# Kernel tuning notes

Hardware: AMD Instinct MI355X
Metric: run time of the kernel (lower is better)

## Reference

```python
import jax, jax.numpy as jnp
import numpy as np

QBITS = 8
QMIN, QMAX = -(2 ** (QBITS - 1)), 2 ** (QBITS - 1) - 1  # qint8: -128..127


def fq_act(x):
    """Per-tensor affine fake-quant (observer = min/max of tensor), with STE."""
    mn = jnp.minimum(jnp.min(x), 0.0)
    mx = jnp.maximum(jnp.max(x), 0.0)
    scale = jnp.maximum((mx - mn) / (QMAX - QMIN), 1e-8)
    zp = QMIN - jnp.round(mn / scale)
    q = jnp.clip(jnp.round(x / scale) + zp, QMIN, QMAX)
    y = (q - zp) * scale
    return x + jax.lax.stop_gradient(y - x)


def fq_w(w):
    """Per-tensor symmetric weight fake-quant, with STE."""
    scale = jnp.maximum(jnp.max(jnp.abs(w)) / QMAX, 1e-8)
    y = jnp.clip(jnp.round(w / scale), QMIN, QMAX) * scale
    return w + jax.lax.stop_gradient(y - w)


def setup_inputs() -> dict:
    key = jax.random.key(0)
    ks = jax.random.split(key, 8)
    B, T, F, K = 32, 1024, 512, 31
    return {
        "x": jax.random.normal(ks[0], (B, T, F), jnp.float32),
        "ln_scale": jnp.ones((F,), jnp.float32),
        "ln_bias": jnp.zeros((F,), jnp.float32),
        "w1": jax.random.normal(ks[1], (2 * F, F), jnp.float32) * 0.02,
        "b1": jax.random.normal(ks[2], (2 * F,), jnp.float32) * 0.02,
        "dw_w": jax.random.normal(ks[3], (F, 1, K), jnp.float32) * 0.1,
        "dw_b": jax.random.normal(ks[4], (F,), jnp.float32) * 0.02,
        "bn_gamma": jnp.ones((F,), jnp.float32),
        "bn_beta": jnp.zeros((F,), jnp.float32),
        "bn_mean": jnp.zeros((F,), jnp.float32),
        "bn_var": jax.random.uniform(ks[5], (F,), jnp.float32, 0.5, 1.5),
        "w2": jax.random.normal(ks[6], (F, F), jnp.float32) * 0.02,
        "b2": jax.random.normal(ks[7], (F,), jnp.float32) * 0.02,
    }


def reference(x, ln_scale, ln_bias, w1, b1, dw_w, dw_b,
              bn_gamma, bn_beta, bn_mean, bn_var, w2, b2):
    F = x.shape[-1]
    # --- custom L1 layer norm, fake-quant in/out ---
    t = fq_act(x)
    t = t - jnp.mean(t, axis=-1, keepdims=True)
    t = t / (jnp.sum(jnp.abs(t), axis=-1, keepdims=True) / F + 1e-5)
    t = t * ln_scale + ln_bias
    t = fq_act(t)
    # --- pointwise conv 1 (linear F -> 2F), quant-wrapped ---
    t = fq_act(t)
    t = jnp.einsum("btf,of->bto", t, fq_w(w1)) + b1
    t = fq_act(t)
    # --- GLU, quant-wrapped ---
    t = fq_act(t)
    a, g = jnp.split(t, 2, axis=-1)
    t = a * jax.nn.sigmoid(g)
    t = fq_act(t)
    # --- depthwise conv over time, quant-wrapped ---
    t = jnp.transpose(t, (0, 2, 1))  # [B,F,T]
    t = fq_act(t)
    t = jax.lax.conv_general_dilated(
        t, fq_w(dw_w), window_strides=(1,), padding=[((dw_w.shape[-1] - 1) // 2,) * 2],
        dimension_numbers=("NCH", "OIH", "NCH"), feature_group_count=F,
    ) + dw_b[:, None]
    t = fq_act(t)
    # --- batch norm (eval mode, running stats), quant-wrapped ---
    t = fq_act(t)
    t = (t - bn_mean[:, None]) * (bn_gamma[:, None] / jnp.sqrt(bn_var[:, None] + 1e-5)) + bn_beta[:, None]
    t = fq_act(t)
    t = jnp.transpose(t, (0, 2, 1))  # [B,T,F]
    # --- SiLU activation, quant-wrapped ---
    t = fq_act(t)
    t = jax.nn.silu(t)
    t = fq_act(t)
    # --- pointwise conv 2 (linear F -> F), quant-wrapped ---
    t = fq_act(t)
    t = jnp.einsum("btf,of->bto", t, fq_w(w2)) + b2
    t = fq_act(t)
    return t  # dropout is identity at eval
```

## Files before the change

kernel.cpp:

```cpp
#include <hip/hip_runtime.h>
#include <stdint.h>
#include <math.h>

#define INF __builtin_inff()

typedef __attribute__((ext_vector_type(4))) float f32x4;
typedef __attribute__((ext_vector_type(2))) float f32x2;
typedef __attribute__((ext_vector_type(8))) short s16x8;

#define S_XMN 0
#define S_XMX 1
#define S_T1MN 2
#define S_T1MX 3
#define S_T4MN 4
#define S_T4MX 5
#define S_T7MN 6
#define S_T7MX 7
#define S_CVMN 8
#define S_CVMX 9
#define S_BNMN 10
#define S_BNMX 11
#define S_SIMN 12
#define S_SIMX 13
#define S_T18MN 14
#define S_T18MX 15
#define S_W1 16
#define S_W2 17
#define S_DW 18
#define NSLOT 19

#define NTOT 16777216L
#define TP 1056

__device__ __forceinline__ unsigned enc(float f) {
  unsigned u = __float_as_uint(f);
  return (u & 0x80000000u) ? ~u : (u | 0x80000000u);
}
__device__ __forceinline__ float dec(unsigned k) {
  return (k & 0x80000000u) ? __uint_as_float(k & 0x7FFFFFFFu) : __uint_as_float(~k);
}

struct FQ { float s, zp; };

__device__ __forceinline__ FQ fq_params(float mn_t, float mx_t) {
  float mn = fminf(mn_t, 0.0f), mx = fmaxf(mx_t, 0.0f);
  FQ p;
  p.s = fmaxf((mx - mn) / 255.0f, 1e-8f);
  p.zp = -128.0f - rintf(mn / p.s);
  return p;
}
__device__ __forceinline__ float fq_apply(float x, FQ p) {
  float q = rintf(x / p.s) + p.zp;
  q = fminf(fmaxf(q, -128.0f), 127.0f);
  return (q - p.zp) * p.s;
}
__device__ __forceinline__ float fq_qmz(float x, FQ p) {
  float q = rintf(x / p.s) + p.zp;
  q = fminf(fmaxf(q, -128.0f), 127.0f);
  return q - p.zp;
}
__device__ __forceinline__ void fq_pair(const unsigned* slots, int idx, FQ& p1, FQ& p2) {
  float mn = dec(slots[idx]), mx = dec(slots[idx + 1]);
  p1 = fq_params(mn, mx);
  float ymn = fq_apply(mn, p1), ymx = fq_apply(mx, p1);
  p2 = fq_params(ymn, ymx);
}
__device__ __forceinline__ unsigned short to_bf16(float v) {
  return (unsigned short)(__float_as_uint(v) >> 16);
}
__device__ __forceinline__ float from_bf16(unsigned short u) {
  return __uint_as_float(((unsigned)u) << 16);
}

__device__ __forceinline__ void mm_block_atomic(float mn, float mx, unsigned* smn, unsigned* smx) {
#pragma unroll
  for (int o = 32; o > 0; o >>= 1) {
    mn = fminf(mn, __shfl_down(mn, o, 64));
    mx = fmaxf(mx, __shfl_down(mx, o, 64));
  }
  __shared__ float rmn[16], rmx[16];
  int lane = threadIdx.x & 63, wid = threadIdx.x >> 6;
  int nw = blockDim.x >> 6;
  __syncthreads();
  if (lane == 0) { rmn[wid] = mn; rmx[wid] = mx; }
  __syncthreads();
  if (threadIdx.x == 0) {
    for (int i = 1; i < nw; ++i) { mn = fminf(mn, rmn[i]); mx = fmaxf(mx, rmx[i]); }
    atomicMin(smn, enc(mn));
    atomicMax(smx, enc(mx));
  }
}

__global__ void k_init(unsigned* __restrict__ slots) {
  int i = threadIdx.x;
  if (i < NSLOT) {
    unsigned v;
    if (i < 16) v = (i & 1) ? enc(-INF) : enc(INF);
    else v = enc(0.0f);
    slots[i] = v;
  }
}

__global__ __launch_bounds__(256) void k_redmm(const float* __restrict__ x, unsigned* __restrict__ slots) {
  long i = ((long)blockIdx.x * 256 + threadIdx.x) * 4;
  const long stride = (long)2048 * 256 * 4;
  float mn = INF, mx = -INF;
  for (; i < NTOT; i += stride) {
    f32x4 v = *(const f32x4*)(x + i);
    mn = fminf(mn, fminf(fminf(v.x, v.y), fminf(v.z, v.w)));
    mx = fmaxf(mx, fmaxf(fmaxf(v.x, v.y), fmaxf(v.z, v.w)));
  }
  mm_block_atomic(mn, mx, slots + S_XMN, slots + S_XMX);
}

__global__ __launch_bounds__(256) void k_wabs(const float* __restrict__ w1, const float* __restrict__ w2,
                                              const float* __restrict__ dw, unsigned* __restrict__ slots) {
  int b = blockIdx.x;
  const float* p; int slot; long base;
  if (b < 2048) { p = w1; slot = S_W1; base = (long)b * 256; }
  else if (b < 3072) { p = w2; slot = S_W2; base = (long)(b - 2048) * 256; }
  else { p = dw; slot = S_DW; base = (long)(b - 3072) * 256; }
  float v = fabsf(p[base + threadIdx.x]);
#pragma unroll
  for (int o = 32; o > 0; o >>= 1) v = fmaxf(v, __shfl_down(v, o, 64));
  __shared__ float r[4];
  int lane = threadIdx.x & 63, wid = threadIdx.x >> 6;
  if (lane == 0) r[wid] = v;
  __syncthreads();
  if (threadIdx.x == 0) {
    v = fmaxf(fmaxf(r[0], r[1]), fmaxf(r[2], r[3]));
    atomicMax(slots + slot, enc(v));
  }
}

__global__ __launch_bounds__(256) void k_wq(const float* __restrict__ w1, const float* __restrict__ w2,
    const float* __restrict__ dw, unsigned short* __restrict__ w1q, unsigned short* __restrict__ w2q,
    float* __restrict__ dwq, const unsigned* __restrict__ slots) {
  int b = blockIdx.x;
  if (b < 2048) {
    float s = fmaxf(dec(slots[S_W1]) / 127.0f, 1e-8f);
    long i = (long)b * 256 + threadIdx.x;
    float q = fminf(fmaxf(rintf(w1[i] / s), -128.0f), 127.0f);
    w1q[i] = to_bf16(q);
  } else if (b < 3072) {
    float s = fmaxf(dec(slots[S_W2]) / 127.0f, 1e-8f);
    long i = (long)(b - 2048) * 256 + threadIdx.x;
    float q = fminf(fmaxf(rintf(w2[i] / s), -128.0f), 127.0f);
    w2q[i] = to_bf16(q);
  } else {
    float s = fmaxf(dec(slots[S_DW]) / 127.0f, 1e-8f);
    long i = (long)(b - 3072) * 256 + threadIdx.x;
    float q = fminf(fmaxf(rintf(dw[i] / s), -128.0f), 127.0f);
    dwq[i] = q;
  }
}

__device__ __forceinline__ float block_sum256(float v, float* sh) {
#pragma unroll
  for (int o = 32; o > 0; o >>= 1) v += __shfl_down(v, o, 64);
  int lane = threadIdx.x & 63, wid = threadIdx.x >> 6;
  __syncthreads();
  if (lane == 0) sh[wid] = v;
  __syncthreads();
  return sh[0] + sh[1] + sh[2] + sh[3];
}

__global__ __launch_bounds__(256) void k_ln(const float* __restrict__ x, const float* __restrict__ lns,
    const float* __restrict__ lnb, float* __restrict__ t1, unsigned* __restrict__ slots) {
  __shared__ float sh[4];
  FQ p0 = fq_params(dec(slots[S_XMN]), dec(slots[S_XMX]));
  int c = threadIdx.x * 2;
  f32x2 sc = *(const f32x2*)(lns + c);
  f32x2 bi = *(const f32x2*)(lnb + c);
  float lmn = INF, lmx = -INF;
  for (int rr = 0; rr < 16; ++rr) {
    long row = (long)blockIdx.x * 16 + rr;
    const float* xr = x + row * 512;
    f32x2 xv = *(const f32x2*)(xr + c);
    float a0 = fq_apply(xv.x, p0), a1 = fq_apply(xv.y, p0);
    float mean = block_sum256(a0 + a1, sh) / 512.0f;
    a0 -= mean; a1 -= mean;
    float denom = block_sum256(fabsf(a0) + fabsf(a1), sh) / 512.0f + 1e-5f;
    a0 = (a0 / denom) * sc.x + bi.x;
    a1 = (a1 / denom) * sc.y + bi.y;
    f32x2 o; o.x = a0; o.y = a1;
    *(f32x2*)(t1 + row * 512 + c) = o;
    lmn = fminf(lmn, fminf(a0, a1));
    lmx = fmaxf(lmx, fmaxf(a0, a1));
  }
  mm_block_atomic(lmn, lmx, slots + S_T1MN, slots + S_T1MX);
}

__global__ __launch_bounds__(256) void k_qa(const float* __restrict__ t1, unsigned short* __restrict__ A1,
                                            const unsigned* __restrict__ slots) {
  FQ p1, p2; fq_pair(slots, S_T1MN, p1, p2);
  long i = ((long)blockIdx.x * 256 + threadIdx.x) * 8;
  const long stride = (long)2048 * 256 * 8;
  for (; i < NTOT; i += stride) {
    f32x4 v0 = *(const f32x4*)(t1 + i);
    f32x4 v1 = *(const f32x4*)(t1 + i + 4);
    s16x8 o;
#pragma unroll
    for (int j = 0; j < 4; ++j) o[j] = (short)to_bf16(fq_qmz(fq_apply(v0[j], p1), p2));
#pragma unroll
    for (int j = 0; j < 4; ++j) o[j + 4] = (short)to_bf16(fq_qmz(fq_apply(v1[j], p1), p2));
    *(s16x8*)(A1 + i) = o;
  }
}

__global__ __launch_bounds__(256) void k_gemm(const unsigned short* __restrict__ A,
    const unsigned short* __restrict__ Bm, const float* __restrict__ bias,
    float* __restrict__ C, int N, unsigned* __restrict__ slots, int mmIdx, int wIdx, int omIdx) {
  __shared__ __align__(16) unsigned short lA[128 * 64];
  __shared__ __align__(16) unsigned short lB[128 * 64];
  FQ p1, p2; fq_pair(slots, mmIdx, p1, p2);
  float sw = fmaxf(dec(slots[wIdx]) / 127.0f, 1e-8f);
  float sAB = p2.s * sw;
  int tid = threadIdx.x;
  int m0 = blockIdx.y * 128, n0 = blockIdx.x * 128;
  int lane = tid & 63, wid = tid >> 6;
  int wm = (wid >> 1) * 64, wn = (wid & 1) * 64;
  const f32x4 fz = {0.0f, 0.0f, 0.0f, 0.0f};
  f32x4 acc[4][4];
#pragma unroll
  for (int mi = 0; mi < 4; ++mi)
#pragma unroll
    for (int ni = 0; ni < 4; ++ni) acc[mi][ni] = fz;
  int sr = tid >> 1;
  int scu = (tid & 1) * 32;
  int swz = (sr & 7) * 8;
  const unsigned short* Ag = A + (long)(m0 + sr) * 512 + scu;
  const unsigned short* Bg = Bm + (long)(n0 + sr) * 512 + scu;
  int fr = lane & 15;
  int fc = (lane >> 4) * 8;
  for (int kt = 0; kt < 8; ++kt) {
    s16x8 ra[4], rb[4];
#pragma unroll
    for (int j = 0; j < 4; ++j) {
      ra[j] = *(const s16x8*)(Ag + kt * 64 + j * 8);
      rb[j] = *(const s16x8*)(Bg + kt * 64 + j * 8);
    }
    __syncthreads();
#pragma unroll
    for (int j = 0; j < 4; ++j) {
      *(s16x8*)&lA[sr * 64 + ((scu + j * 8) ^ swz)] = ra[j];
      *(s16x8*)&lB[sr * 64 + ((scu + j * 8) ^ swz)] = rb[j];
    }
    __syncthreads();
#pragma unroll
    for (int ks = 0; ks < 2; ++ks) {
      s16x8 af[4], bfv[4];
#pragma unroll
      for (int mi = 0; mi < 4; ++mi) {
        int r = wm + mi * 16 + fr;
        af[mi] = *(const s16x8*)&lA[r * 64 + ((ks * 32 + fc) ^ ((r & 7) * 8))];
      }
#pragma unroll
      for (int ni = 0; ni < 4; ++ni) {
        int r = wn + ni * 16 + fr;
        bfv[ni] = *(const s16x8*)&lB[r * 64 + ((ks * 32 + fc) ^ ((r & 7) * 8))];
      }
#pragma unroll
      for (int mi = 0; mi < 4; ++mi)
#pragma unroll
        for (int ni = 0; ni < 4; ++ni)
          acc[mi][ni] = __builtin_amdgcn_mfma_f32_16x16x32_bf16(af[mi], bfv[ni], acc[mi][ni], 0, 0, 0);
    }
  }
  float lmn = INF, lmx = -INF;
  int rb0 = m0 + wm + ((lane >> 4) << 2);
  int cb0 = n0 + wn + (lane & 15);
#pragma unroll
  for (int mi = 0; mi < 4; ++mi) {
#pragma unroll
    for (int ni = 0; ni < 4; ++ni) {
      int col = cb0 + ni * 16;
      float bv = bias[col];
#pragma unroll
      for (int r = 0; r < 4; ++r) {
        int rowi = rb0 + mi * 16 + r;
        float v = sAB * acc[mi][ni][r] + bv;
        C[(long)rowi * N + col] = v;
        lmn = fminf(lmn, v); lmx = fmaxf(lmx, v);
      }
    }
  }
  mm_block_atomic(lmn, lmx, slots + omIdx, slots + omIdx + 1);
}

__global__ __launch_bounds__(256) void k_glu(const float* __restrict__ t4, float* __restrict__ t7,
                                             unsigned* __restrict__ slots) {
  FQ p1, p2; fq_pair(slots, S_T4MN, p1, p2);
  long i = ((long)blockIdx.x * 256 + threadIdx.x) * 4;
  const long stride = (long)2048 * 256 * 4;
  float lmn = INF, lmx = -INF;
  for (; i < NTOT; i += stride) {
    long r = i >> 9;
    int c = (int)(i & 511);
    const float* pa = t4 + r * 1024 + c;
    f32x4 av = *(const f32x4*)pa;
    f32x4 gv = *(const f32x4*)(pa + 512);
    f32x4 o;
#pragma unroll
    for (int j = 0; j < 4; ++j) {
      float a = fq_apply(fq_apply(av[j], p1), p2);
      float g = fq_apply(fq_apply(gv[j], p1), p2);
      float y = a * (1.0f / (1.0f + expf(-g)));
      o[j] = y;
      lmn = fminf(lmn, y); lmx = fmaxf(lmx, y);
    }
    *(f32x4*)(t7 + i) = o;
  }
  mm_block_atomic(lmn, lmx, slots + S_T7MN, slots + S_T7MX);
}

__global__ void k_qt(const float* __restrict__ t7, unsigned short* __restrict__ vT,
                     const unsigned* __restrict__ slots) {
  FQ p1, p2; fq_pair(slots, S_T7MN, p1, p2);
  int b = blockIdx.z, fg = blockIdx.y, tq = blockIdx.x;
  int f = fg * 64 + threadIdx.x;
  const float* in = t7 + (long)b * 1024 * 512 + f;
  unsigned short* orow = vT + (long)(b * 512 + f) * TP + 16;
  for (int tt = 0; tt < 256; tt += 8) {
    int tbase = tq * 256 + tt;
    s16x8 o;
#pragma unroll
    for (int j = 0; j < 8; ++j) {
      float v = in[(long)(tbase + j) * 512];
      o[j] = (short)to_bf16(fq_qmz(fq_apply(v, p1), p2));
    }
    *(s16x8*)(orow + tbase) = o;
  }
  s16x8 z = {0, 0, 0, 0, 0, 0, 0, 0};
  if (tq == 0) { *(s16x8*)(orow - 16) = z; *(s16x8*)(orow - 8) = z; }
  if (tq == 3) { *(s16x8*)(orow + 1024) = z; *(s16x8*)(orow + 1032) = z; }
}

__global__ __launch_bounds__(256) void k_conv(const unsigned short* __restrict__ vT,
    const float* __restrict__ dwq, const float* __restrict__ dwb,
    float* __restrict__ out, unsigned* __restrict__ slots) {
  FQ pC, pD; fq_pair(slots, S_T7MN, pC, pD);
  float sdw = fmaxf(dec(slots[S_DW]) / 127.0f, 1e-8f);
  float scv = pD.s * sdw;
  int b = blockIdx.y;
  int f = blockIdx.x * 8 + (threadIdx.x >> 5);
  int tbase = (threadIdx.x & 31) * 32;
  float w[31];
#pragma unroll
  for (int k = 0; k < 31; ++k) w[k] = dwq[f * 31 + k];
  float bias = dwb[f];
  const unsigned short* row = vT + (long)(b * 512 + f) * TP + 16;
  float* orow = out + (long)(b * 512 + f) * 1024;
  float lmn = INF, lmx = -INF;
  for (int half = 0; half < 2; ++half) {
    int t0 = tbase + half * 16;
    float win[48];
#pragma unroll
    for (int cch = 0; cch < 6; ++cch) {
      s16x8 u = *(const s16x8*)(row + t0 - 16 + cch * 8);
#pragma unroll
      for (int j = 0; j < 8; ++j) win[cch * 8 + j] = from_bf16((unsigned short)u[j]);
    }
#pragma unroll
    for (int tt = 0; tt < 16; tt += 4) {
      f32x4 o;
#pragma unroll
      for (int q = 0; q < 4; ++q) {
        float acc = 0.0f;
#pragma unroll
        for (int k = 0; k < 31; ++k) acc += win[tt + q + 1 + k] * w[k];
        float v = scv * acc + bias;
        o[q] = v;
        lmn = fminf(lmn, v); lmx = fmaxf(lmx, v);
      }
      *(f32x4*)(orow + t0 + tt) = o;
    }
  }
  mm_block_atomic(lmn, lmx, slots + S_CVMN, slots + S_CVMX);
}

__global__ __launch_bounds__(256) void k_bn(const float* __restrict__ in,
    const float* __restrict__ gm, const float* __restrict__ bt,
    const float* __restrict__ mu, const float* __restrict__ vr,
    float* __restrict__ out, unsigned* __restrict__ slots) {
  FQ p1, p2; fq_pair(slots, S_CVMN, p1, p2);
  long i = ((long)blockIdx.x * 256 + threadIdx.x) * 4;
  const long stride = (long)2048 * 256 * 4;
  float lmn = INF, lmx = -INF;
  for (; i < NTOT; i += stride) {
    int f = (int)((i >> 10) & 511);
    float g = gm[f] / sqrtf(vr[f] + 1e-5f);
    float m = mu[f], be = bt[f];
    f32x4 v = *(const f32x4*)(in + i);
    f32x4 o;
#pragma unroll
    for (int j = 0; j < 4; ++j) {
      float y = fq_apply(fq_apply(v[j], p1), p2);
      float r2 = (y - m) * g + be;
      o[j] = r2;
      lmn = fminf(lmn, r2); lmx = fmaxf(lmx, r2);
    }
    *(f32x4*)(out + i) = o;
  }
  mm_block_atomic(lmn, lmx, slots + S_BNMN, slots + S_BNMX);
}

__global__ __launch_bounds__(256) void k_silu(const float* __restrict__ in, float* __restrict__ out,
                                              unsigned* __restrict__ slots) {
  FQ p1, p2; fq_pair(slots, S_BNMN, p1, p2);
  long i = ((long)blockIdx.x * 256 + threadIdx.x) * 4;
  const long stride = (long)2048 * 256 * 4;
  float lmn = INF, lmx = -INF;
  for (; i < NTOT; i += stride) {
    f32x4 v = *(const f32x4*)(in + i);
    f32x4 o;
#pragma unroll
    for (int j = 0; j < 4; ++j) {
      float y = fq_apply(fq_apply(v[j], p1), p2);
      float r2 = y * (1.0f / (1.0f + expf(-y)));
      o[j] = r2;
      lmn = fminf(lmn, r2); lmx = fmaxf(lmx, r2);
    }
    *(f32x4*)(out + i) = o;
  }
  mm_block_atomic(lmn, lmx, slots + S_SIMN, slots + S_SIMX);
}

__global__ void k_q2t(const float* __restrict__ si, unsigned short* __restrict__ A2,
                      const unsigned* __restrict__ slots) {
  FQ p1, p2; fq_pair(slots, S_SIMN, p1, p2);
  int b = blockIdx.z;
  int t = blockIdx.y * 64 + threadIdx.x;
  int fc0 = blockIdx.x * 128;
  const float* in = si + (long)b * 512 * 1024 + t;
  unsigned short* orow = A2 + (long)(b * 1024 + t) * 512;
  for (int fc = 0; fc < 128; fc += 8) {
    int f = fc0 + fc;
    s16x8 o;
#pragma unroll
    for (int j = 0; j < 8; ++j) {
      float v = in[(long)(f + j) * 1024];
      o[j] = (short)to_bf16(fq_qmz(fq_apply(v, p1), p2));
    }
    *(s16x8*)(orow + f) = o;
  }
}

__global__ __launch_bounds__(256) void k_final(const float* __restrict__ t18, float* __restrict__ out,
                                               const unsigned* __restrict__ slots) {
  FQ p = fq_params(dec(slots[S_T18MN]), dec(slots[S_T18MX]));
  long i = ((long)blockIdx.x * 256 + threadIdx.x) * 4;
  const long stride = (long)2048 * 256 * 4;
  for (; i < NTOT; i += stride) {
    f32x4 v = *(const f32x4*)(t18 + i);
    f32x4 o;
#pragma unroll
    for (int j = 0; j < 4; ++j) o[j] = fq_apply(v[j], p);
    *(f32x4*)(out + i) = o;
  }
}

extern "C" void kernel_launch(void* const* d_in, const int* in_sizes, int n_in,
                              void* d_out, int out_size, void* d_ws, size_t ws_size,
                              hipStream_t stream) {
  const float* x   = (const float*)d_in[0];
  const float* lns = (const float*)d_in[1];
  const float* lnb = (const float*)d_in[2];
  const float* w1  = (const float*)d_in[3];
  const float* b1  = (const float*)d_in[4];
  const float* dw  = (const float*)d_in[5];
  const float* dwb = (const float*)d_in[6];
  const float* gm  = (const float*)d_in[7];
  const float* bt  = (const float*)d_in[8];
  const float* mu  = (const float*)d_in[9];
  const float* vr  = (const float*)d_in[10];
  const float* w2  = (const float*)d_in[11];
  const float* b2  = (const float*)d_in[12];
  float* out = (float*)d_out;
  char* ws = (char*)d_ws;

  const size_t OFF_B = 134217728;
  const size_t OFF_D = OFF_B + 67108864;
  const size_t OFF_W = OFF_D + 34603008;
  const size_t NEED = OFF_W + 1048576 + 524288 + 63488 + 256;
  if (ws_size < NEED) return;

  float* t1    = (float*)ws;
  float* t4    = (float*)ws;
  float* half2 = (float*)(ws + 67108864);
  float* bufB  = (float*)(ws + OFF_B);
  unsigned short* bufD = (unsigned short*)(ws + OFF_D);
  unsigned short* w1q = (unsigned short*)(ws + OFF_W);
  unsigned short* w2q = (unsigned short*)(ws + OFF_W + 1048576);
  float* dwq = (float*)(ws + OFF_W + 1048576 + 524288);
  unsigned* slots = (unsigned*)(ws + OFF_W + 1048576 + 524288 + 63488);

  k_init<<<1, 32, 0, stream>>>(slots);
  k_redmm<<<2048, 256, 0, stream>>>(x, slots);
  k_wabs<<<3134, 256, 0, stream>>>(w1, w2, dw, slots);
  k_wq<<<3134, 256, 0, stream>>>(w1, w2, dw, w1q, w2q, dwq, slots);
  k_ln<<<2048, 256, 0, stream>>>(x, lns, lnb, t1, slots);
  k_qa<<<2048, 256, 0, stream>>>(t1, bufD, slots);
  k_gemm<<<dim3(8, 256), 256, 0, stream>>>(bufD, w1q, b1, t4, 1024, slots, S_T1MN, S_W1, S_T4MN);
  k_glu<<<2048, 256, 0, stream>>>(t4, bufB, slots);
  k_qt<<<dim3(4, 8, 32), 64, 0, stream>>>(bufB, bufD, slots);
  k_conv<<<dim3(64, 32), 256, 0, stream>>>(bufD, dwq, dwb, bufB, slots);
  k_bn<<<2048, 256, 0, stream>>>(bufB, gm, bt, mu, vr, half2, slots);
  k_silu<<<2048, 256, 0, stream>>>(half2, bufB, slots);
  k_q2t<<<dim3(4, 16, 32), 64, 0, stream>>>(bufB, bufD, slots);
  k_gemm<<<dim3(4, 256), 256, 0, stream>>>(bufD, w2q, b2, half2, 512, slots, S_SIMN, S_W2, S_T18MN);
  k_final<<<2048, 256, 0, stream>>>(half2, out, slots);
}
```

Baseline: 823.5 us.

## Recompute LN/BN/SiLU chains instead of materializing intermediates; conv in [B,T,F] layout

Stops writing the layer-norm output and the BN/SiLU intermediates to memory. Each later pass recomputes the chain from the source tensor: LN from x in both the min/max pass and the quantize pass, and BN and SiLU from the conv output in three passes. The depthwise conv now reads the GLU output directly in [B,T,F] layout with per-thread column windows and writes [B,T,F], which removes both transpose kernels and the padded bf16 buffer. BN gamma/sqrt(var) is precomputed once in the init kernel. The cost is extra recomputation, including repeated expf and block reductions, and strided per-thread conv loads in exchange for less DRAM traffic.

```diff
diff --git a/kernel.cpp b/kernel.cpp
--- a/kernel.cpp
+++ b/kernel.cpp
@@ -7,6 +7,7 @@
 typedef __attribute__((ext_vector_type(4))) float f32x4;
 typedef __attribute__((ext_vector_type(2))) float f32x2;
 typedef __attribute__((ext_vector_type(8))) short s16x8;
+typedef __attribute__((ext_vector_type(4))) short s16x4;
 
 #define S_XMN 0
 #define S_XMX 1
@@ -30,7 +31,6 @@
 #define NSLOT 19
 
 #define NTOT 16777216L
-#define TP 1056
 
 __device__ __forceinline__ unsigned enc(float f) {
   unsigned u = __float_as_uint(f);
@@ -91,14 +91,11 @@
   }
 }
 
-__global__ void k_init(unsigned* __restrict__ slots) {
+__global__ void k_init(unsigned* __restrict__ slots, const float* __restrict__ gm,
+                       const float* __restrict__ vr, float* __restrict__ gs) {
   int i = threadIdx.x;
-  if (i < NSLOT) {
-    unsigned v;
-    if (i < 16) v = (i & 1) ? enc(-INF) : enc(INF);
-    else v = enc(0.0f);
-    slots[i] = v;
-  }
+  if (i < NSLOT) slots[i] = (i < 16) ? ((i & 1) ? enc(-INF) : enc(INF)) : enc(0.0f);
+  gs[i] = gm[i] / sqrtf(vr[i] + 1e-5f);
 }
 
 __global__ __launch_bounds__(256) void k_redmm(const float* __restrict__ x, unsigned* __restrict__ slots) {
@@ -165,8 +162,21 @@
   return sh[0] + sh[1] + sh[2] + sh[3];
 }
 
-__global__ __launch_bounds__(256) void k_ln(const float* __restrict__ x, const float* __restrict__ lns,
-    const float* __restrict__ lnb, float* __restrict__ t1, unsigned* __restrict__ slots) {
+__device__ __forceinline__ f32x2 ln_row(const float* __restrict__ xr, int c, FQ p0,
+                                        f32x2 sc, f32x2 bi, float* sh) {
+  f32x2 xv = *(const f32x2*)(xr + c);
+  float a0 = fq_apply(xv.x, p0), a1 = fq_apply(xv.y, p0);
+  float mean = block_sum256(a0 + a1, sh) / 512.0f;
+  a0 -= mean; a1 -= mean;
+  float denom = block_sum256(fabsf(a0) + fabsf(a1), sh) / 512.0f + 1e-5f;
+  f32x2 o;
+  o.x = (a0 / denom) * sc.x + bi.x;
+  o.y = (a1 / denom) * sc.y + bi.y;
+  return o;
+}
+
+__global__ __launch_bounds__(256) void k_lnmm(const float* __restrict__ x, const float* __restrict__ lns,
+    const float* __restrict__ lnb, unsigned* __restrict__ slots) {
   __shared__ float sh[4];
   FQ p0 = fq_params(dec(slots[S_XMN]), dec(slots[S_XMX]));
   int c = threadIdx.x * 2;
@@ -175,36 +185,27 @@
   float lmn = INF, lmx = -INF;
   for (int rr = 0; rr < 16; ++rr) {
     long row = (long)blockIdx.x * 16 + rr;
-    const float* xr = x + row * 512;
-    f32x2 xv = *(const f32x2*)(xr + c);
-    float a0 = fq_apply(xv.x, p0), a1 = fq_apply(xv.y, p0);
-    float mean = block_sum256(a0 + a1, sh) / 512.0f;
-    a0 -= mean; a1 -= mean;
-    float denom = block_sum256(fabsf(a0) + fabsf(a1), sh) / 512.0f + 1e-5f;
-    a0 = (a0 / denom) * sc.x + bi.x;
-    a1 = (a1 / denom) * sc.y + bi.y;
-    f32x2 o; o.x = a0; o.y = a1;
-    *(f32x2*)(t1 + row * 512 + c) = o;
-    lmn = fminf(lmn, fminf(a0, a1));
-    lmx = fmaxf(lmx, fmaxf(a0, a1));
+    f32x2 a = ln_row(x + row * 512, c, p0, sc, bi, sh);
+    lmn = fminf(lmn, fminf(a.x, a.y));
+    lmx = fmaxf(lmx, fmaxf(a.x, a.y));
   }
   mm_block_atomic(lmn, lmx, slots + S_T1MN, slots + S_T1MX);
 }
 
-__global__ __launch_bounds__(256) void k_qa(const float* __restrict__ t1, unsigned short* __restrict__ A1,
-                                            const unsigned* __restrict__ slots) {
+__global__ __launch_bounds__(256) void k_qa(const float* __restrict__ x, const float* __restrict__ lns,
+    const float* __restrict__ lnb, unsigned short* __restrict__ A1, const unsigned* __restrict__ slots) {
+  __shared__ float sh[4];
+  FQ p0 = fq_params(dec(slots[S_XMN]), dec(slots[S_XMX]));
   FQ p1, p2; fq_pair(slots, S_T1MN, p1, p2);
-  long i = ((long)blockIdx.x * 256 + threadIdx.x) * 8;
-  const long stride = (long)2048 * 256 * 8;
-  for (; i < NTOT; i += stride) {
-    f32x4 v0 = *(const f32x4*)(t1 + i);
-    f32x4 v1 = *(const f32x4*)(t1 + i + 4);
-    s16x8 o;
-#pragma unroll
-    for (int j = 0; j < 4; ++j) o[j] = (short)to_bf16(fq_qmz(fq_apply(v0[j], p1), p2));
-#pragma unroll
-    for (int j = 0; j < 4; ++j) o[j + 4] = (short)to_bf16(fq_qmz(fq_apply(v1[j], p1), p2));
-    *(s16x8*)(A1 + i) = o;
+  int c = threadIdx.x * 2;
+  f32x2 sc = *(const f32x2*)(lns + c);
+  f32x2 bi = *(const f32x2*)(lnb + c);
+  for (int rr = 0; rr < 16; ++rr) {
+    long row = (long)blockIdx.x * 16 + rr;
+    f32x2 a = ln_row(x + row * 512, c, p0, sc, bi, sh);
+    unsigned pk = (unsigned)to_bf16(fq_qmz(fq_apply(a.x, p1), p2))
+                | ((unsigned)to_bf16(fq_qmz(fq_apply(a.y, p1), p2)) << 16);
+    *(unsigned*)(A1 + row * 512 + c) = pk;
   }
 }
 
@@ -314,135 +315,115 @@
   mm_block_atomic(lmn, lmx, slots + S_T7MN, slots + S_T7MX);
 }
 
-__global__ void k_qt(const float* __restrict__ t7, unsigned short* __restrict__ vT,
-                     const unsigned* __restrict__ slots) {
-  FQ p1, p2; fq_pair(slots, S_T7MN, p1, p2);
-  int b = blockIdx.z, fg = blockIdx.y, tq = blockIdx.x;
-  int f = fg * 64 + threadIdx.x;
-  const float* in = t7 + (long)b * 1024 * 512 + f;
-  unsigned short* orow = vT + (long)(b * 512 + f) * TP + 16;
-  for (int tt = 0; tt < 256; tt += 8) {
-    int tbase = tq * 256 + tt;
-    s16x8 o;
-#pragma unroll
-    for (int j = 0; j < 8; ++j) {
-      float v = in[(long)(tbase + j) * 512];
-      o[j] = (short)to_bf16(fq_qmz(fq_apply(v, p1), p2));
-    }
-    *(s16x8*)(orow + tbase) = o;
-  }
-  s16x8 z = {0, 0, 0, 0, 0, 0, 0, 0};
-  if (tq == 0) { *(s16x8*)(orow - 16) = z; *(s16x8*)(orow - 8) = z; }
-  if (tq == 3) { *(s16x8*)(orow + 1024) = z; *(s16x8*)(orow + 1032) = z; }
-}
-
-__global__ __launch_bounds__(256) void k_conv(const unsigned short* __restrict__ vT,
+__global__ __launch_bounds__(256) void k_conv(const float* __restrict__ t7,
     const float* __restrict__ dwq, const float* __restrict__ dwb,
     float* __restrict__ out, unsigned* __restrict__ slots) {
-  FQ pC, pD; fq_pair(slots, S_T7MN, pC, pD);
+  FQ p1, p2; fq_pair(slots, S_T7MN, p1, p2);
   float sdw = fmaxf(dec(slots[S_DW]) / 127.0f, 1e-8f);
-  float scv = pD.s * sdw;
-  int b = blockIdx.y;
-  int f = blockIdx.x * 8 + (threadIdx.x >> 5);
-  int tbase = (threadIdx.x & 31) * 32;
-  float w[31];
-#pragma unroll
-  for (int k = 0; k < 31; ++k) w[k] = dwq[f * 31 + k];
+  float scv = p2.s * sdw;
+  int t0 = blockIdx.x * 32;
+  int f = blockIdx.y * 256 + threadIdx.x;
+  int b = blockIdx.z;
+  const float* base = t7 + (long)b * 1024 * 512 + f;
+  float col[62];
+#pragma unroll
+  for (int r = 0; r < 62; ++r) {
+    int t = t0 - 15 + r;
+    float q = 0.0f;
+    if ((unsigned)t < 1024u) q = fq_qmz(fq_apply(base[(long)t * 512], p1), p2);
+    col[r] = q;
+  }
+  float w31[31];
+#pragma unroll
+  for (int k = 0; k < 31; ++k) w31[k] = dwq[f * 31 + k];
   float bias = dwb[f];
-  const unsigned short* row = vT + (long)(b * 512 + f) * TP + 16;
-  float* orow = out + (long)(b * 512 + f) * 1024;
-  float lmn = INF, lmx = -INF;
-  for (int half = 0; half < 2; ++half) {
-    int t0 = tbase + half * 16;
-    float win[48];
-#pragma unroll
-    for (int cch = 0; cch < 6; ++cch) {
-      s16x8 u = *(const s16x8*)(row + t0 - 16 + cch * 8);
-#pragma unroll
-      for (int j = 0; j < 8; ++j) win[cch * 8 + j] = from_bf16((unsigned short)u[j]);
-    }
-#pragma unroll
-    for (int tt = 0; tt < 16; tt += 4) {
-      f32x4 o;
-#pragma unroll
-      for (int q = 0; q < 4; ++q) {
-        float acc = 0.0f;
-#pragma unroll
-        for (int k = 0; k < 31; ++k) acc += win[tt + q + 1 + k] * w[k];
-        float v = scv * acc + bias;
-        o[q] = v;
-        lmn = fminf(lmn, v); lmx = fmaxf(lmx, v);
-      }
-      *(f32x4*)(orow + t0 + tt) = o;
-    }
+  float* orow = out + ((long)b * 1024 + t0) * 512 + f;
+  float lmn = INF, lmx = -INF;
+#pragma unroll
+  for (int j = 0; j < 32; ++j) {
+    float acc = 0.0f;
+#pragma unroll
+    for (int k = 0; k < 31; ++k) acc += col[j + k] * w31[k];
+    float v = scv * acc + bias;
+    lmn = fminf(lmn, v); lmx = fmaxf(lmx, v);
+    orow[(long)j * 512] = v;
   }
   mm_block_atomic(lmn, lmx, slots + S_CVMN, slots + S_CVMX);
 }
 
-__global__ __launch_bounds__(256) void k_bn(const float* __restrict__ in,
-    const float* __restrict__ gm, const float* __restrict__ bt,
-    const float* __restrict__ mu, const float* __restrict__ vr,
-    float* __restrict__ out, unsigned* __restrict__ slots) {
-  FQ p1, p2; fq_pair(slots, S_CVMN, p1, p2);
-  long i = ((long)blockIdx.x * 256 + threadIdx.x) * 4;
-  const long stride = (long)2048 * 256 * 4;
-  float lmn = INF, lmx = -INF;
-  for (; i < NTOT; i += stride) {
-    int f = (int)((i >> 10) & 511);
-    float g = gm[f] / sqrtf(vr[f] + 1e-5f);
-    float m = mu[f], be = bt[f];
-    f32x4 v = *(const f32x4*)(in + i);
-    f32x4 o;
-#pragma unroll
-    for (int j = 0; j < 4; ++j) {
-      float y = fq_apply(fq_apply(v[j], p1), p2);
-      float r2 = (y - m) * g + be;
-      o[j] = r2;
+__device__ __forceinline__ float bn_val(float v, FQ c1, FQ c2, float gsv, float muv, float btv) {
+  float y = fq_apply(fq_apply(v, c1), c2);
+  return (y - muv) * gsv + btv;
+}
+
+__global__ __launch_bounds__(256) void k_bnmm(const float* __restrict__ conv,
+    const float* __restrict__ gs, const float* __restrict__ mu, const float* __restrict__ bt,
+    unsigned* __restrict__ slots) {
+  FQ c1, c2; fq_pair(slots, S_CVMN, c1, c2);
+  long i = ((long)blockIdx.x * 256 + threadIdx.x) * 4;
+  const long stride = (long)2048 * 256 * 4;
+  float lmn = INF, lmx = -INF;
+  for (; i < NTOT; i += stride) {
+    int f0 = (int)(i & 511);
+    f32x4 v = *(const f32x4*)(conv + i);
+    f32x4 g4 = *(const f32x4*)(gs + f0);
+    f32x4 m4 = *(const f32x4*)(mu + f0);
+    f32x4 b4 = *(const f32x4*)(bt + f0);
+#pragma unroll
+    for (int j = 0; j < 4; ++j) {
+      float r2 = bn_val(v[j], c1, c2, g4[j], m4[j], b4[j]);
       lmn = fminf(lmn, r2); lmx = fmaxf(lmx, r2);
     }
-    *(f32x4*)(out + i) = o;
   }
   mm_block_atomic(lmn, lmx, slots + S_BNMN, slots + S_BNMX);
 }
 
-__global__ __launch_bounds__(256) void k_silu(const float* __restrict__ in, float* __restrict__ out,
-                                              unsigned* __restrict__ slots) {
-  FQ p1, p2; fq_pair(slots, S_BNMN, p1, p2);
-  long i = ((long)blockIdx.x * 256 + threadIdx.x) * 4;
-  const long stride = (long)2048 * 256 * 4;
-  float lmn = INF, lmx = -INF;
-  for (; i < NTOT; i += stride) {
-    f32x4 v = *(const f32x4*)(in + i);
-    f32x4 o;
-#pragma unroll
-    for (int j = 0; j < 4; ++j) {
-      float y = fq_apply(fq_apply(v[j], p1), p2);
-      float r2 = y * (1.0f / (1.0f + expf(-y)));
-      o[j] = r2;
-      lmn = fminf(lmn, r2); lmx = fmaxf(lmx, r2);
-    }
-    *(f32x4*)(out + i) = o;
+__global__ __launch_bounds__(256) void k_silumm(const float* __restrict__ conv,
+    const float* __restrict__ gs, const float* __restrict__ mu, const float* __restrict__ bt,
+    unsigned* __restrict__ slots) {
+  FQ c1, c2; fq_pair(slots, S_CVMN, c1, c2);
+  FQ b1q, b2q; fq_pair(slots, S_BNMN, b1q, b2q);
+  long i = ((long)blockIdx.x * 256 + threadIdx.x) * 4;
+  const long stride = (long)2048 * 256 * 4;
+  float lmn = INF, lmx = -INF;
+  for (; i < NTOT; i += stride) {
+    int f0 = (int)(i & 511);
+    f32x4 v = *(const f32x4*)(conv + i);
+    f32x4 g4 = *(const f32x4*)(gs + f0);
+    f32x4 m4 = *(const f32x4*)(mu + f0);
+    f32x4 b4 = *(const f32x4*)(bt + f0);
+#pragma unroll
+    for (int j = 0; j < 4; ++j) {
+      float z = fq_apply(fq_apply(bn_val(v[j], c1, c2, g4[j], m4[j], b4[j]), b1q), b2q);
+      float si = z * (1.0f / (1.0f + expf(-z)));
+      lmn = fminf(lmn, si); lmx = fmaxf(lmx, si);
+    }
   }
   mm_block_atomic(lmn, lmx, slots + S_SIMN, slots + S_SIMX);
 }
 
-__global__ void k_q2t(const float* __restrict__ si, unsigned short* __restrict__ A2,
-                      const unsigned* __restrict__ slots) {
-  FQ p1, p2; fq_pair(slots, S_SIMN, p1, p2);
-  int b = blockIdx.z;
-  int t = blockIdx.y * 64 + threadIdx.x;
-  int fc0 = blockIdx.x * 128;
-  const float* in = si + (long)b * 512 * 1024 + t;
-  unsigned short* orow = A2 + (long)(b * 1024 + t) * 512;
-  for (int fc = 0; fc < 128; fc += 8) {
-    int f = fc0 + fc;
-    s16x8 o;
-#pragma unroll
-    for (int j = 0; j < 8; ++j) {
-      float v = in[(long)(f + j) * 1024];
-      o[j] = (short)to_bf16(fq_qmz(fq_apply(v, p1), p2));
-    }
-    *(s16x8*)(orow + f) = o;
+__global__ __launch_bounds__(256) void k_q2(const float* __restrict__ conv,
+    const float* __restrict__ gs, const float* __restrict__ mu, const float* __restrict__ bt,
+    unsigned short* __restrict__ A2, const unsigned* __restrict__ slots) {
+  FQ c1, c2; fq_pair(slots, S_CVMN, c1, c2);
+  FQ b1q, b2q; fq_pair(slots, S_BNMN, b1q, b2q);
+  FQ s1, s2; fq_pair(slots, S_SIMN, s1, s2);
+  long i = ((long)blockIdx.x * 256 + threadIdx.x) * 4;
+  const long stride = (long)2048 * 256 * 4;
+  for (; i < NTOT; i += stride) {
+    int f0 = (int)(i & 511);
+    f32x4 v = *(const f32x4*)(conv + i);
+    f32x4 g4 = *(const f32x4*)(gs + f0);
+    f32x4 m4 = *(const f32x4*)(mu + f0);
+    f32x4 b4 = *(const f32x4*)(bt + f0);
+    s16x4 o;
+#pragma unroll
+    for (int j = 0; j < 4; ++j) {
+      float z = fq_apply(fq_apply(bn_val(v[j], c1, c2, g4[j], m4[j], b4[j]), b1q), b2q);
+      float si = z * (1.0f / (1.0f + expf(-z)));
+      o[j] = (short)to_bf16(fq_qmz(fq_apply(si, s1), s2));
+    }
+    *(s16x4*)(A2 + i) = o;
   }
 }
 
@@ -481,33 +462,31 @@
 
   const size_t OFF_B = 134217728;
   const size_t OFF_D = OFF_B + 67108864;
-  const size_t OFF_W = OFF_D + 34603008;
-  const size_t NEED = OFF_W + 1048576 + 524288 + 63488 + 256;
+  const size_t OFF_W = OFF_D + 33554432;
+  const size_t NEED = OFF_W + 1048576 + 524288 + 63488 + 2048 + 256;
   if (ws_size < NEED) return;
 
-  float* t1    = (float*)ws;
-  float* t4    = (float*)ws;
-  float* half2 = (float*)(ws + 67108864);
-  float* bufB  = (float*)(ws + OFF_B);
+  float* buf0 = (float*)ws;
+  float* bufB = (float*)(ws + OFF_B);
   unsigned short* bufD = (unsigned short*)(ws + OFF_D);
   unsigned short* w1q = (unsigned short*)(ws + OFF_W);
   unsigned short* w2q = (unsigned short*)(ws + OFF_W + 1048576);
   float* dwq = (float*)(ws + OFF_W + 1048576 + 524288);
-  unsigned* slots = (unsigned*)(ws + OFF_W + 1048576 + 524288 + 63488);
-
-  k_init<<<1, 32, 0, stream>>>(slots);
+  float* gs  = (float*)(ws + OFF_W + 1048576 + 524288 + 63488);
+  unsigned* slots = (unsigned*)(ws + OFF_W + 1048576 + 524288 + 63488 + 2048);
+
+  k_init<<<1, 512, 0, stream>>>(slots, gm, vr, gs);
   k_redmm<<<2048, 256, 0, stream>>>(x, slots);
   k_wabs<<<3134, 256, 0, stream>>>(w1, w2, dw, slots);
   k_wq<<<3134, 256, 0, stream>>>(w1, w2, dw, w1q, w2q, dwq, slots);
-  k_ln<<<2048, 256, 0, stream>>>(x, lns, lnb, t1, slots);
-  k_qa<<<2048, 256, 0, stream>>>(t1, bufD, slots);
-  k_gemm<<<dim3(8, 256), 256, 0, stream>>>(bufD, w1q, b1, t4, 1024, slots, S_T1MN, S_W1, S_T4MN);
-  k_glu<<<2048, 256, 0, stream>>>(t4, bufB, slots);
-  k_qt<<<dim3(4, 8, 32), 64, 0, stream>>>(bufB, bufD, slots);
-  k_conv<<<dim3(64, 32), 256, 0, stream>>>(bufD, dwq, dwb, bufB, slots);
-  k_bn<<<2048, 256, 0, stream>>>(bufB, gm, bt, mu, vr, half2, slots);
-  k_silu<<<2048, 256, 0, stream>>>(half2, bufB, slots);
-  k_q2t<<<dim3(4, 16, 32), 64, 0, stream>>>(bufB, bufD, slots);
-  k_gemm<<<dim3(4, 256), 256, 0, stream>>>(bufD, w2q, b2, half2, 512, slots, S_SIMN, S_W2, S_T18MN);
-  k_final<<<2048, 256, 0, stream>>>(half2, out, slots);
-}
+  k_lnmm<<<2048, 256, 0, stream>>>(x, lns, lnb, slots);
+  k_qa<<<2048, 256, 0, stream>>>(x, lns, lnb, bufD, slots);
+  k_gemm<<<dim3(8, 256), 256, 0, stream>>>(bufD, w1q, b1, buf0, 1024, slots, S_T1MN, S_W1, S_T4MN);
+  k_glu<<<2048, 256, 0, stream>>>(buf0, bufB, slots);
+  k_conv<<<dim3(32, 2, 32), 256, 0, stream>>>(bufB, dwq, dwb, buf0, slots);
+  k_bnmm<<<2048, 256, 0, stream>>>(buf0, gs, mu, bt, slots);
+  k_silumm<<<2048, 256, 0, stream>>>(buf0, gs, mu, bt, slots);
+  k_q2<<<2048, 256, 0, stream>>>(buf0, gs, mu, bt, bufD, slots);
+  k_gemm<<<dim3(4, 256), 256, 0, stream>>>(bufD, w2q, b2, bufB, 512, slots, S_SIMN, S_W2, S_T18MN);
+  k_final<<<2048, 256, 0, stream>>>(bufB, out, slots);
+}
```

After: 801.6 us. 2.7% less time.
